# Kernel tuning notes

Hardware: AMD Instinct MI355X
Metric: run time of the kernel (lower is better)

The kernel has to match this reference:

```python
import jax, jax.numpy as jnp
import numpy as np

N_NODES = 100000
N_EDGES = 1600000


def gcn_conv(x, src, dst, W, b, n_nodes):
    # GCNConv: linear transform, then symmetrically-normalized scatter-add
    # (self-loops already appended to src/dst by caller)
    h = x @ W  # [N, out]
    ones = jnp.ones(src.shape[0], dtype=x.dtype)
    deg = jax.ops.segment_sum(ones, dst, num_segments=n_nodes)  # in-degree incl. self-loop
    dinv = jnp.where(deg > 0, jax.lax.rsqrt(deg), jnp.zeros_like(deg))
    norm = dinv[src] * dinv[dst]  # [E]
    out = jax.ops.segment_sum(norm[:, None] * h[src], dst, num_segments=n_nodes)
    return out + b


def setup_inputs() -> dict:
    key = jax.random.key(0)
    ks = jax.random.split(key, 8)
    in_ch, nhid, out_ch = 128, 48, 32
    x = jax.random.normal(ks[0], (N_NODES, in_ch), dtype=jnp.float32)
    edge_index = jax.random.randint(ks[1], (2, N_EDGES), 0, N_NODES, dtype=jnp.int64)
    s1 = 1.0 / np.sqrt(in_ch)
    s2 = 1.0 / np.sqrt(nhid)
    W1 = jax.random.uniform(ks[2], (in_ch, nhid), jnp.float32, -s1, s1)
    b1 = jnp.zeros((nhid,), jnp.float32)
    Wmu = jax.random.uniform(ks[3], (nhid, out_ch), jnp.float32, -s2, s2)
    bmu = jnp.zeros((out_ch,), jnp.float32)
    Wls = jax.random.uniform(ks[4], (nhid, out_ch), jnp.float32, -s2, s2)
    bls = jnp.zeros((out_ch,), jnp.float32)
    return {"x": x, "edge_index": edge_index, "W1": W1, "b1": b1,
            "Wmu": Wmu, "bmu": bmu, "Wls": Wls, "bls": bls}


def reference(x, edge_index, W1, b1, Wmu, bmu, Wls, bls):
    n = x.shape[0]
    loop = jnp.arange(n, dtype=edge_index.dtype)
    src = jnp.concatenate([edge_index[0], loop])
    dst = jnp.concatenate([edge_index[1], loop])
    h = jax.nn.relu(gcn_conv(x, src, dst, W1, b1, n))
    mu = gcn_conv(h, src, dst, Wmu, bmu, n)
    logstd = gcn_conv(h, src, dst, Wls, bls, n)
    return mu, logstd
```

## Files before the change

### kernel.cpp

```cpp
#include <hip/hip_runtime.h>

#define NN 100000
#define NE 1600000
#define FIN 128
#define FH 48
#define FO 32
#define NODES_PER_BLOCK 21

#define LB 7
#define BKT_NODES 128
#define NBKT ((NN + BKT_NODES - 1) / BKT_NODES)
#define PBLK 256
#define EPB (NE / PBLK)


__global__ __launch_bounds__(256) void p1_hist(const int* __restrict__ dst, int* __restrict__ H) {
  __shared__ int hist[NBKT];
  const int t = threadIdx.x, blk = blockIdx.x;
  for (int i = t; i < NBKT; i += 256) hist[i] = 0;
  __syncthreads();
  const int e0 = blk * EPB;
  for (int k = t; k < EPB; k += 256) atomicAdd(&hist[dst[e0 + k] >> LB], 1);
  __syncthreads();
  for (int i = t; i < NBKT; i += 256) H[blk * NBKT + i] = hist[i];
}

__global__ __launch_bounds__(256) void p1_colscan(int* __restrict__ H, int* __restrict__ tot) {
  int b = blockIdx.x * 256 + threadIdx.x;
  if (b >= NBKT) return;
  int run = 0;
  for (int blk = 0; blk < PBLK; ++blk) {
    int v = H[blk * NBKT + b];
    H[blk * NBKT + b] = run;
    run += v;
  }
  tot[b] = run;
}

__global__ __launch_bounds__(256) void p1_scan(const int* __restrict__ tot, int* __restrict__ base,
                                               int* __restrict__ off) {
  __shared__ int s[256];
  const int t = threadIdx.x;
  int c[4]; int sum = 0;
  #pragma unroll
  for (int k = 0; k < 4; ++k) {
    int idx = 4 * t + k;
    c[k] = (idx < NBKT) ? tot[idx] : 0;
    sum += c[k];
  }
  s[t] = sum;
  __syncthreads();
  for (int o = 1; o < 256; o <<= 1) {
    int v = (t >= o) ? s[t - o] : 0;
    __syncthreads();
    s[t] += v;
    __syncthreads();
  }
  int run = s[t] - sum;
  #pragma unroll
  for (int k = 0; k < 4; ++k) {
    int idx = 4 * t + k;
    if (idx < NBKT) base[idx] = run;
    run += c[k];
  }
  if (t == 255) { base[NBKT] = run; off[NN] = run; }
}

__global__ __launch_bounds__(256) void p1_scatter(const int* __restrict__ src, const int* __restrict__ dst,
                                                  const int* __restrict__ H, const int* __restrict__ base,
                                                  int* __restrict__ pairs) {
  __shared__ int cur[NBKT];
  const int t = threadIdx.x, blk = blockIdx.x;
  for (int i = t; i < NBKT; i += 256) cur[i] = base[i] + H[blk * NBKT + i];
  __syncthreads();
  const int e0 = blk * EPB;
  for (int k = t; k < EPB; k += 256) {
    int d = dst[e0 + k];
    int s = src[e0 + k];
    int b = d >> LB;
    int pos = atomicAdd(&cur[b], 1);
    pairs[pos] = s | ((d & (BKT_NODES - 1)) << 17);
  }
}

__global__ __launch_bounds__(256) void p2_bucket(const int* __restrict__ pairs, const int* __restrict__ base,
                                                 int* __restrict__ csr, int* __restrict__ off,
                                                 float* __restrict__ dinv) {
  __shared__ int cnt[BKT_NODES];
  __shared__ int s[BKT_NODES];
  const int t = threadIdx.x, b = blockIdx.x;
  const int j0 = base[b], j1 = base[b + 1];
  if (t < BKT_NODES) cnt[t] = 0;
  __syncthreads();
  for (int j = j0 + t; j < j1; j += 256) atomicAdd(&cnt[pairs[j] >> 17], 1);
  __syncthreads();
  int myc = 0;
  if (t < BKT_NODES) { myc = cnt[t]; s[t] = myc; }
  __syncthreads();
  for (int o = 1; o < BKT_NODES; o <<= 1) {
    int v = (t >= o && t < BKT_NODES) ? s[t - o] : 0;
    __syncthreads();
    if (t < BKT_NODES) s[t] += v;
    __syncthreads();
  }
  int loc = 0;
  if (t < BKT_NODES) loc = s[t] - myc;
  const int n = b * BKT_NODES + t;
  if (t < BKT_NODES && n < NN) {
    off[n] = j0 + loc;
    dinv[n] = rsqrtf((float)myc + 1.0f);
  }
  __syncthreads();
  if (t < BKT_NODES) s[t] = loc;
  __syncthreads();
  for (int j = j0 + t; j < j1; j += 256) {
    int p = pairs[j];
    int pos = atomicAdd(&s[p >> 17], 1);
    csr[j0 + pos] = p & 0x1FFFF;
  }
}


__global__ __launch_bounds__(256) void k_gemm1(const float* __restrict__ x, const float* __restrict__ W1,
                                               float* __restrict__ t1) {
  __shared__ float xs[64][132];
  __shared__ float ws[FIN][FH];
  const int t = threadIdx.x;
  const int row0 = blockIdx.x * 64;

  for (int i = t; i < FIN * FH; i += 256) ws[i / FH][i % FH] = W1[i];
  for (int i = t; i < 64 * (FIN / 4); i += 256) {
    int r = i >> 5, c4 = i & 31;
    float4 v = make_float4(0.f, 0.f, 0.f, 0.f);
    if (row0 + r < NN) v = ((const float4*)x)[(size_t)(row0 + r) * (FIN / 4) + c4];
    xs[r][c4 * 4 + 0] = v.x; xs[r][c4 * 4 + 1] = v.y;
    xs[r][c4 * 4 + 2] = v.z; xs[r][c4 * 4 + 3] = v.w;
  }
  __syncthreads();

  const int row = t >> 2;
  const int cg  = (t & 3) * 12;
  float acc[12];
  #pragma unroll
  for (int j = 0; j < 12; ++j) acc[j] = 0.f;

  #pragma unroll 4
  for (int k = 0; k < FIN; ++k) {
    float xv = xs[row][k];
    const float4* wp = (const float4*)&ws[k][cg];
    float4 w0 = wp[0], w1 = wp[1], w2 = wp[2];
    acc[0] += xv * w0.x; acc[1] += xv * w0.y; acc[2]  += xv * w0.z; acc[3]  += xv * w0.w;
    acc[4] += xv * w1.x; acc[5] += xv * w1.y; acc[6]  += xv * w1.z; acc[7]  += xv * w1.w;
    acc[8] += xv * w2.x; acc[9] += xv * w2.y; acc[10] += xv * w2.z; acc[11] += xv * w2.w;
  }

  const int grow = row0 + row;
  if (grow < NN) {
    float* tp = t1 + (size_t)grow * FH + cg;
    #pragma unroll
    for (int j = 0; j < 12; ++j) tp[j] = acc[j];
  }
}


__global__ __launch_bounds__(256) void k_gather1(const int* __restrict__ off, const int* __restrict__ csr,
                                                 const float* __restrict__ feat, const float* __restrict__ dinv,
                                                 const float* __restrict__ bias, float* __restrict__ out) {
  const int t = threadIdx.x;
  if (t >= NODES_PER_BLOCK * 12) return;
  const int local = t / 12;
  const int f4 = t - local * 12;
  const int node = blockIdx.x * NODES_PER_BLOCK + local;
  if (node >= NN) return;

  const float4* feat4 = (const float4*)feat;
  const float di = dinv[node];
  const float sn = di * di;
  float4 v = feat4[(size_t)node * 12 + f4];
  float4 acc = make_float4(v.x * sn, v.y * sn, v.z * sn, v.w * sn);

  int j = off[node];
  const int jend = off[node + 1];
  for (; j + 4 <= jend; j += 4) {
    int s0 = csr[j], s1 = csr[j + 1], s2 = csr[j + 2], s3 = csr[j + 3];
    float n0 = dinv[s0] * di, n1 = dinv[s1] * di, n2 = dinv[s2] * di, n3 = dinv[s3] * di;
    float4 v0 = feat4[(size_t)s0 * 12 + f4];
    float4 v1 = feat4[(size_t)s1 * 12 + f4];
    float4 v2 = feat4[(size_t)s2 * 12 + f4];
    float4 v3 = feat4[(size_t)s3 * 12 + f4];
    acc.x += n0 * v0.x; acc.y += n0 * v0.y; acc.z += n0 * v0.z; acc.w += n0 * v0.w;
    acc.x += n1 * v1.x; acc.y += n1 * v1.y; acc.z += n1 * v1.z; acc.w += n1 * v1.w;
    acc.x += n2 * v2.x; acc.y += n2 * v2.y; acc.z += n2 * v2.z; acc.w += n2 * v2.w;
    acc.x += n3 * v3.x; acc.y += n3 * v3.y; acc.z += n3 * v3.z; acc.w += n3 * v3.w;
  }
  for (; j < jend; ++j) {
    int s = csr[j];
    float nv = dinv[s] * di;
    float4 vv = feat4[(size_t)s * 12 + f4];
    acc.x += nv * vv.x; acc.y += nv * vv.y; acc.z += nv * vv.z; acc.w += nv * vv.w;
  }

  const float4 bb = ((const float4*)bias)[f4];
  acc.x = fmaxf(acc.x + bb.x, 0.f);
  acc.y = fmaxf(acc.y + bb.y, 0.f);
  acc.z = fmaxf(acc.z + bb.z, 0.f);
  acc.w = fmaxf(acc.w + bb.w, 0.f);
  ((float4*)out)[(size_t)node * 12 + f4] = acc;
}


__global__ __launch_bounds__(256) void k_gather_gemm2(const int* __restrict__ off, const int* __restrict__ csr,
                                                      const float* __restrict__ feat, const float* __restrict__ dinv,
                                                      const float* __restrict__ Wmu, const float* __restrict__ bmu,
                                                      const float* __restrict__ Wls, const float* __restrict__ bls,
                                                      float* __restrict__ out) {
  __shared__ float wall[FH][2 * FO];
  __shared__ float as2[NODES_PER_BLOCK][FH + 1];
  const int t = threadIdx.x;

  for (int i = t; i < FH * 2 * FO; i += 256) {
    int k = i >> 6, c = i & 63;
    wall[k][c] = (c < FO) ? Wmu[k * FO + c] : Wls[k * FO + (c - FO)];
  }

  const int local = t / 12;
  const int f4 = t - local * 12;
  const int node = blockIdx.x * NODES_PER_BLOCK + local;
  const bool active = (local < NODES_PER_BLOCK) && (node < NN);

  if (active) {
    const float4* feat4 = (const float4*)feat;
    const float di = dinv[node];
    const float sn = di * di;
    float4 v = feat4[(size_t)node * 12 + f4];
    float4 acc = make_float4(v.x * sn, v.y * sn, v.z * sn, v.w * sn);

    int j = off[node];
    const int jend = off[node + 1];
    for (; j + 4 <= jend; j += 4) {
      int s0 = csr[j], s1 = csr[j + 1], s2 = csr[j + 2], s3 = csr[j + 3];
      float n0 = dinv[s0] * di, n1 = dinv[s1] * di, n2 = dinv[s2] * di, n3 = dinv[s3] * di;
      float4 v0 = feat4[(size_t)s0 * 12 + f4];
      float4 v1 = feat4[(size_t)s1 * 12 + f4];
      float4 v2 = feat4[(size_t)s2 * 12 + f4];
      float4 v3 = feat4[(size_t)s3 * 12 + f4];
      acc.x += n0 * v0.x; acc.y += n0 * v0.y; acc.z += n0 * v0.z; acc.w += n0 * v0.w;
      acc.x += n1 * v1.x; acc.y += n1 * v1.y; acc.z += n1 * v1.z; acc.w += n1 * v1.w;
      acc.x += n2 * v2.x; acc.y += n2 * v2.y; acc.z += n2 * v2.z; acc.w += n2 * v2.w;
      acc.x += n3 * v3.x; acc.y += n3 * v3.y; acc.z += n3 * v3.z; acc.w += n3 * v3.w;
    }
    for (; j < jend; ++j) {
      int s = csr[j];
      float nv = dinv[s] * di;
      float4 vv = feat4[(size_t)s * 12 + f4];
      acc.x += nv * vv.x; acc.y += nv * vv.y; acc.z += nv * vv.z; acc.w += nv * vv.w;
    }

    float* ap = &as2[local][f4 * 4];
    ap[0] = acc.x; ap[1] = acc.y; ap[2] = acc.z; ap[3] = acc.w;
  }
  __syncthreads();

  for (int o = t; o < NODES_PER_BLOCK * 2 * FO; o += 256) {
    const int ln = o >> 6;
    const int c = o & 63;
    const int grow = blockIdx.x * NODES_PER_BLOCK + ln;
    if (grow < NN) {
      float a = (c < FO) ? bmu[c] : bls[c - FO];
      #pragma unroll
      for (int k = 0; k < FH; ++k) a += as2[ln][k] * wall[k][c];
      if (c < FO) out[(size_t)grow * FO + c] = a;
      else        out[(size_t)NN * FO + (size_t)grow * FO + (c - FO)] = a;
    }
  }
}


extern "C" void kernel_launch(void* const* d_in, const int* in_sizes, int n_in,
                              void* d_out, int out_size, void* d_ws, size_t ws_size,
                              hipStream_t stream) {
  const float* x   = (const float*)d_in[0];
  const int*   ei  = (const int*)d_in[1];
  const float* W1  = (const float*)d_in[2];
  const float* b1  = (const float*)d_in[3];
  const float* Wmu = (const float*)d_in[4];
  const float* bmu = (const float*)d_in[5];
  const float* Wls = (const float*)d_in[6];
  const float* bls = (const float*)d_in[7];
  float* out = (float*)d_out;

  const int* src = ei;
  const int* dst = ei + NE;

  char* base_p = (char*)d_ws;
  int*   pairs = (int*)base_p;
  int*   csr   = pairs + (size_t)NE;
  float* t1    = (float*)(csr + (size_t)NE);
  float* h     = t1 + (size_t)NN * FH;
  int*   H     = (int*)(h + (size_t)NN * FH);
  int*   tot   = H + (size_t)PBLK * NBKT;
  int*   bkb   = tot + NBKT;
  int*   off   = bkb + NBKT + 1;
  float* dinv  = (float*)(off + NN + 1);

  p1_hist   <<<PBLK, 256, 0, stream>>>(dst, H);
  p1_colscan<<<(NBKT + 255) / 256, 256, 0, stream>>>(H, tot);
  p1_scan   <<<1, 256, 0, stream>>>(tot, bkb, off);
  p1_scatter<<<PBLK, 256, 0, stream>>>(src, dst, H, bkb, pairs);
  p2_bucket <<<NBKT, 256, 0, stream>>>(pairs, bkb, csr, off, dinv);

  k_gemm1<<<(NN + 63) / 64, 256, 0, stream>>>(x, W1, t1);
  k_gather1<<<(NN + NODES_PER_BLOCK - 1) / NODES_PER_BLOCK, 256, 0, stream>>>(off, csr, t1, dinv, b1, h);

  k_gather_gemm2<<<(NN + NODES_PER_BLOCK - 1) / NODES_PER_BLOCK, 256, 0, stream>>>(
      off, csr, h, dinv, Wmu, bmu, Wls, bls, out);
}
```

Baseline: 336.4 us.

## Vectorize edge loads, reorder bucket offsets by XCD, stage bucket pairs in LDS

The histogram and scatter passes now read src/dst as int4 with 250 blocks, so each block's edge slice divides evenly into 4-wide loads. The column scan assigns bucket offsets in XCD-interleaved block order, which places each XCD's writes next to each other in the pairs array. p2_bucket copies a bucket's pairs into a 4096-entry LDS staging buffer once and reads them from there in both the counting pass and the placement pass. Buckets larger than the buffer fall back to global reads. The LDS use may lower occupancy.

```diff
diff --git a/kernel.cpp b/kernel.cpp
--- a/kernel.cpp
+++ b/kernel.cpp
@@ -10,17 +10,25 @@
 #define LB 7
 #define BKT_NODES 128
 #define NBKT ((NN + BKT_NODES - 1) / BKT_NODES)
-#define PBLK 256
+#define PBLK 250
 #define EPB (NE / PBLK)
-
-
-__global__ __launch_bounds__(256) void p1_hist(const int* __restrict__ dst, int* __restrict__ H) {
+#define EPB4 (EPB / 4)
+#define P2CAP 4096
+
+
+__global__ __launch_bounds__(256) void p1_hist(const int4* __restrict__ dst4, int* __restrict__ H) {
   __shared__ int hist[NBKT];
   const int t = threadIdx.x, blk = blockIdx.x;
   for (int i = t; i < NBKT; i += 256) hist[i] = 0;
   __syncthreads();
-  const int e0 = blk * EPB;
-  for (int k = t; k < EPB; k += 256) atomicAdd(&hist[dst[e0 + k] >> LB], 1);
+  const int k0 = blk * EPB4;
+  for (int k = t; k < EPB4; k += 256) {
+    int4 d = dst4[k0 + k];
+    atomicAdd(&hist[d.x >> LB], 1);
+    atomicAdd(&hist[d.y >> LB], 1);
+    atomicAdd(&hist[d.z >> LB], 1);
+    atomicAdd(&hist[d.w >> LB], 1);
+  }
   __syncthreads();
   for (int i = t; i < NBKT; i += 256) H[blk * NBKT + i] = hist[i];
 }
@@ -29,10 +37,12 @@
   int b = blockIdx.x * 256 + threadIdx.x;
   if (b >= NBKT) return;
   int run = 0;
-  for (int blk = 0; blk < PBLK; ++blk) {
-    int v = H[blk * NBKT + b];
-    H[blk * NBKT + b] = run;
-    run += v;
+  for (int xcd = 0; xcd < 8; ++xcd) {
+    for (int blk = xcd; blk < PBLK; blk += 8) {
+      int v = H[blk * NBKT + b];
+      H[blk * NBKT + b] = run;
+      run += v;
+    }
   }
   tot[b] = run;
 }
@@ -66,33 +76,50 @@
   if (t == 255) { base[NBKT] = run; off[NN] = run; }
 }
 
-__global__ __launch_bounds__(256) void p1_scatter(const int* __restrict__ src, const int* __restrict__ dst,
+__global__ __launch_bounds__(256) void p1_scatter(const int4* __restrict__ src4, const int4* __restrict__ dst4,
                                                   const int* __restrict__ H, const int* __restrict__ base,
                                                   int* __restrict__ pairs) {
   __shared__ int cur[NBKT];
   const int t = threadIdx.x, blk = blockIdx.x;
   for (int i = t; i < NBKT; i += 256) cur[i] = base[i] + H[blk * NBKT + i];
   __syncthreads();
-  const int e0 = blk * EPB;
-  for (int k = t; k < EPB; k += 256) {
-    int d = dst[e0 + k];
-    int s = src[e0 + k];
-    int b = d >> LB;
-    int pos = atomicAdd(&cur[b], 1);
-    pairs[pos] = s | ((d & (BKT_NODES - 1)) << 17);
+  const int k0 = blk * EPB4;
+  for (int k = t; k < EPB4; k += 256) {
+    int4 s = src4[k0 + k];
+    int4 d = dst4[k0 + k];
+    int b0 = d.x >> LB, b1 = d.y >> LB, b2 = d.z >> LB, b3 = d.w >> LB;
+    int p0 = atomicAdd(&cur[b0], 1);
+    pairs[p0] = s.x | ((d.x & (BKT_NODES - 1)) << 17);
+    int p1 = atomicAdd(&cur[b1], 1);
+    pairs[p1] = s.y | ((d.y & (BKT_NODES - 1)) << 17);
+    int p2 = atomicAdd(&cur[b2], 1);
+    pairs[p2] = s.z | ((d.z & (BKT_NODES - 1)) << 17);
+    int p3 = atomicAdd(&cur[b3], 1);
+    pairs[p3] = s.w | ((d.w & (BKT_NODES - 1)) << 17);
   }
 }
 
 __global__ __launch_bounds__(256) void p2_bucket(const int* __restrict__ pairs, const int* __restrict__ base,
                                                  int* __restrict__ csr, int* __restrict__ off,
                                                  float* __restrict__ dinv) {
+  __shared__ int stage[P2CAP];
   __shared__ int cnt[BKT_NODES];
   __shared__ int s[BKT_NODES];
   const int t = threadIdx.x, b = blockIdx.x;
   const int j0 = base[b], j1 = base[b + 1];
+  const int ne = j1 - j0;
+  const bool fits = (ne <= P2CAP);
+
   if (t < BKT_NODES) cnt[t] = 0;
-  __syncthreads();
-  for (int j = j0 + t; j < j1; j += 256) atomicAdd(&cnt[pairs[j] >> 17], 1);
+  if (fits) {
+    for (int j = t; j < ne; j += 256) stage[j] = pairs[j0 + j];
+  }
+  __syncthreads();
+  if (fits) {
+    for (int j = t; j < ne; j += 256) atomicAdd(&cnt[stage[j] >> 17], 1);
+  } else {
+    for (int j = j0 + t; j < j1; j += 256) atomicAdd(&cnt[pairs[j] >> 17], 1);
+  }
   __syncthreads();
   int myc = 0;
   if (t < BKT_NODES) { myc = cnt[t]; s[t] = myc; }
@@ -113,10 +140,18 @@
   __syncthreads();
   if (t < BKT_NODES) s[t] = loc;
   __syncthreads();
-  for (int j = j0 + t; j < j1; j += 256) {
-    int p = pairs[j];
-    int pos = atomicAdd(&s[p >> 17], 1);
-    csr[j0 + pos] = p & 0x1FFFF;
+  if (fits) {
+    for (int j = t; j < ne; j += 256) {
+      int p = stage[j];
+      int pos = atomicAdd(&s[p >> 17], 1);
+      csr[j0 + pos] = p & 0x1FFFF;
+    }
+  } else {
+    for (int j = j0 + t; j < j1; j += 256) {
+      int p = pairs[j];
+      int pos = atomicAdd(&s[p >> 17], 1);
+      csr[j0 + pos] = p & 0x1FFFF;
+    }
   }
 }
 
@@ -289,8 +324,8 @@
   const float* bls = (const float*)d_in[7];
   float* out = (float*)d_out;
 
-  const int* src = ei;
-  const int* dst = ei + NE;
+  const int4* src4 = (const int4*)ei;
+  const int4* dst4 = (const int4*)(ei + NE);
 
   char* base_p = (char*)d_ws;
   int*   pairs = (int*)base_p;
@@ -303,10 +338,10 @@
   int*   off   = bkb + NBKT + 1;
   float* dinv  = (float*)(off + NN + 1);
 
-  p1_hist   <<<PBLK, 256, 0, stream>>>(dst, H);
+  p1_hist   <<<PBLK, 256, 0, stream>>>(dst4, H);
   p1_colscan<<<(NBKT + 255) / 256, 256, 0, stream>>>(H, tot);
   p1_scan   <<<1, 256, 0, stream>>>(tot, bkb, off);
-  p1_scatter<<<PBLK, 256, 0, stream>>>(src, dst, H, bkb, pairs);
+  p1_scatter<<<PBLK, 256, 0, stream>>>(src4, dst4, H, bkb, pairs);
   p2_bucket <<<NBKT, 256, 0, stream>>>(pairs, bkb, csr, off, dinv);
 
   k_gemm1<<<(NN + 63) / 64, 256, 0, stream>>>(x, W1, t1);
```

New measurement: 320.2 us. 4.8% less time.
